# Kernel tuning notes

Hardware: AMD Instinct MI355X
Metric: run time of the kernel (lower is better)

The kernel has to match this reference:

```python
import jax, jax.numpy as jnp
import numpy as np

B, T, E, D = 8, 2048, 1024, 64  # batch, seq_len, n_emb, head_dim

def setup_inputs() -> dict:
    key = jax.random.key(0)
    ks = jax.random.split(key, 4)
    scale = 1.0 / np.sqrt(E)
    return {
        "x": jax.random.normal(ks[0], (B, T, E), dtype=jnp.float32),
        "Wq": jax.random.normal(ks[1], (E, D), dtype=jnp.float32) * scale,
        "bq": jnp.zeros((D,), dtype=jnp.float32),
        "Wk": jax.random.normal(ks[2], (E, D), dtype=jnp.float32) * scale,
        "bk": jnp.zeros((D,), dtype=jnp.float32),
        "Wv": jax.random.normal(ks[3], (E, D), dtype=jnp.float32) * scale,
        "bv": jnp.zeros((D,), dtype=jnp.float32),
    }

def reference(x, Wq, bq, Wk, bk, Wv, bv):
    # QKV projections: [B,T,E] @ [E,D] -> [B,T,D]
    q = x @ Wq + bq
    k = x @ Wk + bk
    v = x @ Wv + bv
    d = q.shape[-1]
    # scaled dot-product scores [B,T,T]
    wei = jnp.einsum('btd,bsd->bts', q, k) * (d ** -0.5)
    # causal mask: position t attends to s <= t
    t = wei.shape[1]
    causal = jnp.tril(jnp.ones((t, t), dtype=bool))
    wei = jnp.where(causal, wei, -jnp.inf)
    wei = jax.nn.softmax(wei, axis=-1)
    # attention output [B,T,D]
    return jnp.einsum('bts,bsd->btd', wei, v)
```

## Files before the change

### kernel.cpp

```cpp
#include <hip/hip_runtime.h>
#include <math.h>


#define B_   8
#define T_   2048
#define E_   1024
#define D_   64
#define BT_  (B_ * T_)

typedef __attribute__((ext_vector_type(8))) short s16x8;
typedef __attribute__((ext_vector_type(4))) short s16x4;
typedef __attribute__((ext_vector_type(4))) float f32x4;

__device__ __forceinline__ short f2bf(float f) {
    union { float f; unsigned u; } a; a.f = f;
    unsigned r = a.u + 0x7fffu + ((a.u >> 16) & 1u);
    return (short)(r >> 16);
}

#define MFMA16(a, b, c) __builtin_amdgcn_mfma_f32_16x16x32_bf16((a), (b), (c), 0, 0, 0)

#define DPPF(x, ctrl) __builtin_bit_cast(float, \
    __builtin_amdgcn_update_dpp(0, __builtin_bit_cast(int, (x)), (ctrl), 0xF, 0xF, true))

__device__ __forceinline__ float rsum16(float x) {
    x += DPPF(x, 0xB1);
    x += DPPF(x, 0x4E);
    x += DPPF(x, 0x124);
    x += DPPF(x, 0x128);
    return x;
}

__global__ __launch_bounds__(256) void wtrans_kernel(
    const float* __restrict__ Wq, const float* __restrict__ Wk,
    const float* __restrict__ Wv, short* __restrict__ Wt)
{
    __shared__ float sT[64][65];
    const int sel = blockIdx.x >> 4;
    const int k0  = (blockIdx.x & 15) * 64;
    const float* W = sel == 0 ? Wq : (sel == 1 ? Wk : Wv);
    const int t  = threadIdx.x;
    const int kr = t >> 4, c4 = (t & 15) * 4;
    #pragma unroll
    for (int i = 0; i < 4; ++i) {
        float4 v = *(const float4*)&W[(size_t)(k0 + kr + i * 16) * D_ + c4];
        sT[kr + i * 16][c4 + 0] = v.x; sT[kr + i * 16][c4 + 1] = v.y;
        sT[kr + i * 16][c4 + 2] = v.z; sT[kr + i * 16][c4 + 3] = v.w;
    }
    __syncthreads();
    #pragma unroll
    for (int i = 0; i < 4; ++i) {
        int n  = (t >> 4) + i * 16;
        int kk = (t & 15) * 4;
        s16x4 o;
        o.x = f2bf(sT[kk + 0][n]); o.y = f2bf(sT[kk + 1][n]);
        o.z = f2bf(sT[kk + 2][n]); o.w = f2bf(sT[kk + 3][n]);
        *(s16x4*)&Wt[(size_t)(sel * 64 + n) * E_ + k0 + kk] = o;
    }
}

__global__ __launch_bounds__(256) void qkv_kernel(
    const float* __restrict__ x, const short* __restrict__ Wt,
    const float* __restrict__ bq, const float* __restrict__ bk,
    const float* __restrict__ bv,
    short* __restrict__ Qg, short* __restrict__ Kg, short* __restrict__ VTg)
{
    __shared__ short sX[2][32 * 76];
    const int tid  = threadIdx.x;
    const int lane = tid & 63;
    const int w    = tid >> 6;
    const int l15  = lane & 15, quad = lane >> 4;
    const int t0   = blockIdx.x * 32;
    const int bb   = t0 >> 11;

    const int srow = tid >> 3;
    const int skc  = (tid & 7) * 8;
    const float* px = &x[(size_t)(t0 + srow) * E_ + skc];

    f32x4 acc[3][2];
    #pragma unroll
    for (int a = 0; a < 3; ++a)
        #pragma unroll
        for (int h = 0; h < 2; ++h)
            acc[a][h] = (f32x4){0.f, 0.f, 0.f, 0.f};

    float4 lda0 = *(const float4*)px;
    float4 lda1 = *(const float4*)(px + 4);
    float4 ldb0 = *(const float4*)(px + 64);
    float4 ldb1 = *(const float4*)(px + 68);

    int buf = 0;
    for (int k0 = 0; k0 < E_; k0 += 64) {
        s16x8 pk;
        pk[0] = f2bf(lda0.x); pk[1] = f2bf(lda0.y);
        pk[2] = f2bf(lda0.z); pk[3] = f2bf(lda0.w);
        pk[4] = f2bf(lda1.x); pk[5] = f2bf(lda1.y);
        pk[6] = f2bf(lda1.z); pk[7] = f2bf(lda1.w);
        *(s16x8*)&sX[buf][srow * 76 + skc] = pk;
        __syncthreads();

        lda0 = ldb0; lda1 = ldb1;
        if (k0 + 128 < E_) {
            const float* p2 = px + k0 + 128;
            ldb0 = *(const float4*)p2;
            ldb1 = *(const float4*)(p2 + 4);
        }

        s16x8 aw[3][2];
        #pragma unroll
        for (int t3 = 0; t3 < 3; ++t3) {
            const short* pw = &Wt[(size_t)((w * 3 + t3) * 16 + l15) * E_ + k0 + quad * 8];
            aw[t3][0] = *(const s16x8*)pw;
            aw[t3][1] = *(const s16x8*)(pw + 32);
        }
        s16x8 bxf[2][2];
        #pragma unroll
        for (int h = 0; h < 2; ++h) {
            bxf[h][0] = *(const s16x8*)&sX[buf][(h * 16 + l15) * 76 + quad * 8];
            bxf[h][1] = *(const s16x8*)&sX[buf][(h * 16 + l15) * 76 + 32 + quad * 8];
        }
        #pragma unroll
        for (int t3 = 0; t3 < 3; ++t3)
            #pragma unroll
            for (int h = 0; h < 2; ++h) {
                acc[t3][h] = MFMA16(aw[t3][0], bxf[h][0], acc[t3][h]);
                acc[t3][h] = MFMA16(aw[t3][1], bxf[h][1], acc[t3][h]);
            }
        buf ^= 1;
    }

    __syncthreads();
    short* sVT = &sX[0][0];

    #pragma unroll
    for (int t3 = 0; t3 < 3; ++t3) {
        const int nt = w * 3 + t3;
        const int fb = (nt & 3) * 16 + quad * 4;
        const float* bias = nt < 4 ? bq : (nt < 8 ? bk : bv);
        f32x4 bsv = *(const f32x4*)&bias[fb];
        #pragma unroll
        for (int h = 0; h < 2; ++h) {
            const int tok = t0 + h * 16 + l15;
            f32x4 v = acc[t3][h] + bsv;
            if (nt < 4) {
                v *= 0.125f;
                s16x4 o = { f2bf(v[0]), f2bf(v[1]), f2bf(v[2]), f2bf(v[3]) };
                *(s16x4*)&Qg[(size_t)tok * D_ + fb] = o;
            } else if (nt < 8) {
                s16x4 o = { f2bf(v[0]), f2bf(v[1]), f2bf(v[2]), f2bf(v[3]) };
                *(s16x4*)&Kg[(size_t)tok * D_ + fb] = o;
            } else {
                const int lt = h * 16 + l15;
                #pragma unroll
                for (int r = 0; r < 4; ++r)
                    sVT[(fb + r) * 48 + lt] = f2bf(v[r]);
            }
        }
    }
    __syncthreads();
    {
        const int d  = tid >> 2;
        const int tq = (tid & 3) * 8;
        s16x8 vv = *(const s16x8*)&sVT[d * 48 + tq];
        *(s16x8*)&VTg[(size_t)(bb * D_ + d) * T_ + (t0 & (T_ - 1)) + tq] = vv;
    }
}

__global__ __launch_bounds__(256) void attn_kernel(
    const short* __restrict__ Qg, const short* __restrict__ Kg,
    const short* __restrict__ VTg, float* __restrict__ out)
{
    __shared__ char smem[20736];
    short* sP = (short*)smem;
    float* sO = (float*)smem;
    float* sl = (float*)(smem + 20480);

    const int tid  = threadIdx.x;
    const int lane = tid & 63;
    const int w    = tid >> 6;
    const int l15  = lane & 15, quad = lane >> 4;
    const int b    = blockIdx.x & 7;
    const int pr   = blockIdx.x >> 3;
    const int jA   = pr, jB = 127 - pr;
    const int tqA  = jA * 16, tqB = jB * 16;
    const int nchA = (jA >> 2) + 1, nchB = (jB >> 2) + 1;
    const int tot  = nchA + nchB;
    const int seg  = (tot + 3) >> 2;
    const int c0   = w * seg;
    const int c1   = (c0 + seg < tot) ? c0 + seg : tot;

    const size_t qoffA = ((size_t)b * T_ + tqA + l15) * D_ + quad * 8;
    const s16x8 aqA0 = *(const s16x8*)&Qg[qoffA];
    const s16x8 aqA1 = *(const s16x8*)&Qg[qoffA + 32];
    const size_t qoffB = ((size_t)b * T_ + tqB + l15) * D_ + quad * 8;
    const s16x8 aqB0 = *(const s16x8*)&Qg[qoffB];
    const s16x8 aqB1 = *(const s16x8*)&Qg[qoffB + 32];

    f32x4 oA[4], oB[4];
    float lA[4] = {0.f, 0.f, 0.f, 0.f}, lB[4] = {0.f, 0.f, 0.f, 0.f};
    #pragma unroll
    for (int nt = 0; nt < 4; ++nt) {
        oA[nt] = (f32x4){0.f, 0.f, 0.f, 0.f};
        oB[nt] = (f32x4){0.f, 0.f, 0.f, 0.f};
    }

    const short* kb = Kg  + (size_t)b * T_ * D_;
    const short* vb = VTg + (size_t)b * D_ * T_;
    short* sPw = sP + w * (16 * 72);

    auto body = [&](int cc, int tq, int nch, const s16x8& q0, const s16x8& q1,
                    f32x4 (&oo)[4], float (&lp)[4]) {
        const int s0 = cc * 64;
        s16x8 bk[4][2];
        #pragma unroll
        for (int nt = 0; nt < 4; ++nt) {
            const short* pk = kb + (size_t)(s0 + nt * 16 + l15) * D_ + quad * 8;
            bk[nt][0] = *(const s16x8*)pk;
            bk[nt][1] = *(const s16x8*)(pk + 32);
        }
        const f32x4 zz = (f32x4){0.f, 0.f, 0.f, 0.f};
        f32x4 sacc[4];
        #pragma unroll
        for (int nt = 0; nt < 4; ++nt) {
            sacc[nt] = MFMA16(q0, bk[nt][0], zz);
            sacc[nt] = MFMA16(q1, bk[nt][1], sacc[nt]);
        }
        s16x8 bv[4][2];
        #pragma unroll
        for (int nt = 0; nt < 4; ++nt) {
            const short* pv = vb + (size_t)(nt * 16 + l15) * T_ + s0 + quad * 8;
            bv[nt][0] = *(const s16x8*)pv;
            bv[nt][1] = *(const s16x8*)(pv + 32);
        }
        const bool diag = (cc == nch - 1);
        float p[4][4];
        #pragma unroll
        for (int nt = 0; nt < 4; ++nt)
            #pragma unroll
            for (int r = 0; r < 4; ++r) {
                float e = __expf(sacc[nt][r]);
                if (diag && (s0 + nt * 16 + l15 > tq + quad * 4 + r)) e = 0.f;
                p[nt][r] = e;
            }
        #pragma unroll
        for (int r = 0; r < 4; ++r)
            lp[r] += (p[0][r] + p[1][r]) + (p[2][r] + p[3][r]);
        #pragma unroll
        for (int nt = 0; nt < 4; ++nt)
            #pragma unroll
            for (int r = 0; r < 4; ++r)
                sPw[(quad * 4 + r) * 72 + nt * 16 + l15] = f2bf(p[nt][r]);
        s16x8 ap0 = *(const s16x8*)&sPw[l15 * 72 + quad * 8];
        s16x8 ap1 = *(const s16x8*)&sPw[l15 * 72 + 32 + quad * 8];
        #pragma unroll
        for (int nt = 0; nt < 4; ++nt) {
            oo[nt] = MFMA16(ap0, bv[nt][0], oo[nt]);
            oo[nt] = MFMA16(ap1, bv[nt][1], oo[nt]);
        }
    };

    for (int c = c0; c < c1; ++c) {
        if (c < nchA) body(c, tqA, nchA, aqA0, aqA1, oA, lA);
        else          body(c - nchA, tqB, nchB, aqB0, aqB1, oB, lB);
    }

    f32x4 lvA, lvB;
    #pragma unroll
    for (int r = 0; r < 4; ++r) { lvA[r] = rsum16(lA[r]); lvB[r] = rsum16(lB[r]); }

    const int d  = tid & 63;
    const int rb = (tid >> 6) * 4;

    __syncthreads();
    {
        float* sOw = sO + w * (64 * 20);
        #pragma unroll
        for (int nt = 0; nt < 4; ++nt)
            *(f32x4*)&sOw[(nt * 16 + l15) * 20 + quad * 4] = oA[nt];
        if (l15 == 0) *(f32x4*)&sl[w * 16 + quad * 4] = lvA;
    }
    __syncthreads();
    {
        f32x4 osum = (f32x4){0.f, 0.f, 0.f, 0.f};
        f32x4 lsum = (f32x4){0.f, 0.f, 0.f, 0.f};
        #pragma unroll
        for (int w2 = 0; w2 < 4; ++w2) {
            osum += *(const f32x4*)&sO[w2 * (64 * 20) + d * 20 + rb];
            lsum += *(const f32x4*)&sl[w2 * 16 + rb];
        }
        #pragma unroll
        for (int i = 0; i < 4; ++i)
            out[((size_t)b * T_ + tqA + rb + i) * D_ + d] = osum[i] / lsum[i];
    }

    __syncthreads();
    {
        float* sOw = sO + w * (64 * 20);
        #pragma unroll
        for (int nt = 0; nt < 4; ++nt)
            *(f32x4*)&sOw[(nt * 16 + l15) * 20 + quad * 4] = oB[nt];
        if (l15 == 0) *(f32x4*)&sl[w * 16 + quad * 4] = lvB;
    }
    __syncthreads();
    {
        f32x4 osum = (f32x4){0.f, 0.f, 0.f, 0.f};
        f32x4 lsum = (f32x4){0.f, 0.f, 0.f, 0.f};
        #pragma unroll
        for (int w2 = 0; w2 < 4; ++w2) {
            osum += *(const f32x4*)&sO[w2 * (64 * 20) + d * 20 + rb];
            lsum += *(const f32x4*)&sl[w2 * 16 + rb];
        }
        #pragma unroll
        for (int i = 0; i < 4; ++i)
            out[((size_t)b * T_ + tqB + rb + i) * D_ + d] = osum[i] / lsum[i];
    }
}

extern "C" void kernel_launch(void* const* d_in, const int* in_sizes, int n_in,
                              void* d_out, int out_size, void* d_ws, size_t ws_size,
                              hipStream_t stream) {
    (void)in_sizes; (void)n_in; (void)out_size; (void)ws_size;
    const float* x  = (const float*)d_in[0];
    const float* Wq = (const float*)d_in[1];
    const float* bq = (const float*)d_in[2];
    const float* Wk = (const float*)d_in[3];
    const float* bk = (const float*)d_in[4];
    const float* Wv = (const float*)d_in[5];
    const float* bv = (const float*)d_in[6];

    char* ws = (char*)d_ws;
    short* Qg  = (short*)(ws);
    short* Kg  = (short*)(ws + (size_t)2 * 1024 * 1024);
    short* VTg = (short*)(ws + (size_t)4 * 1024 * 1024);
    short* Wt  = (short*)(ws + (size_t)6 * 1024 * 1024);

    wtrans_kernel<<<48, 256, 0, stream>>>(Wq, Wk, Wv, Wt);
    qkv_kernel<<<BT_ / 32, 256, 0, stream>>>(x, Wt, bq, bk, bv, Qg, Kg, VTg);
    attn_kernel<<<B_ * 64, 256, 0, stream>>>(Qg, Kg, VTg, (float*)d_out);
}
```

Measured before the change: 160.7 us.

## Load x fragments directly into registers in QKV projection, drop LDS staging

The QKV projection kernel now processes 16 tokens per block instead of 32. Each lane loads its x fragment straight from global memory in the MFMA operand layout, which removes the shared-memory staging of x and the per-iteration block barrier. The grid doubles and launch bounds request higher occupancy, aiming for more latency hiding. The cost is that each block reads the weight tile for half as many tokens, doubling total weight traffic, though that traffic mostly hits cache.

```diff
diff --git a/kernel.cpp b/kernel.cpp
--- a/kernel.cpp
+++ b/kernel.cpp
@@ -59,78 +59,71 @@
     }
 }
 
-__global__ __launch_bounds__(256) void qkv_kernel(
+__global__ __launch_bounds__(256, 4) void qkv_kernel(
     const float* __restrict__ x, const short* __restrict__ Wt,
     const float* __restrict__ bq, const float* __restrict__ bk,
     const float* __restrict__ bv,
     short* __restrict__ Qg, short* __restrict__ Kg, short* __restrict__ VTg)
 {
-    __shared__ short sX[2][32 * 76];
+    __shared__ short sVT[64 * 24];
     const int tid  = threadIdx.x;
     const int lane = tid & 63;
     const int w    = tid >> 6;
     const int l15  = lane & 15, quad = lane >> 4;
-    const int t0   = blockIdx.x * 32;
+    const int t0   = blockIdx.x * 16;
     const int bb   = t0 >> 11;
 
-    const int srow = tid >> 3;
-    const int skc  = (tid & 7) * 8;
-    const float* px = &x[(size_t)(t0 + srow) * E_ + skc];
-
-    f32x4 acc[3][2];
-    #pragma unroll
-    for (int a = 0; a < 3; ++a)
-        #pragma unroll
-        for (int h = 0; h < 2; ++h)
-            acc[a][h] = (f32x4){0.f, 0.f, 0.f, 0.f};
-
-    float4 lda0 = *(const float4*)px;
-    float4 lda1 = *(const float4*)(px + 4);
-    float4 ldb0 = *(const float4*)(px + 64);
-    float4 ldb1 = *(const float4*)(px + 68);
-
-    int buf = 0;
+    const float* px = &x[(size_t)(t0 + l15) * E_ + quad * 8];
+
+    f32x4 acc[3];
+    #pragma unroll
+    for (int t3 = 0; t3 < 3; ++t3) acc[t3] = (f32x4){0.f, 0.f, 0.f, 0.f};
+
+    float4 a0 = *(const float4*)(px +   0);
+    float4 a1 = *(const float4*)(px +   4);
+    float4 a2 = *(const float4*)(px +  32);
+    float4 a3 = *(const float4*)(px +  36);
+    float4 b0 = *(const float4*)(px +  64);
+    float4 b1 = *(const float4*)(px +  68);
+    float4 b2 = *(const float4*)(px +  96);
+    float4 b3 = *(const float4*)(px + 100);
+
+    const short* pw0 = &Wt[(size_t)((w * 3 + 0) * 16 + l15) * E_ + quad * 8];
+    const short* pw1 = pw0 + (size_t)16 * E_;
+    const short* pw2 = pw1 + (size_t)16 * E_;
+
     for (int k0 = 0; k0 < E_; k0 += 64) {
-        s16x8 pk;
-        pk[0] = f2bf(lda0.x); pk[1] = f2bf(lda0.y);
-        pk[2] = f2bf(lda0.z); pk[3] = f2bf(lda0.w);
-        pk[4] = f2bf(lda1.x); pk[5] = f2bf(lda1.y);
-        pk[6] = f2bf(lda1.z); pk[7] = f2bf(lda1.w);
-        *(s16x8*)&sX[buf][srow * 76 + skc] = pk;
-        __syncthreads();
-
-        lda0 = ldb0; lda1 = ldb1;
+        s16x8 f0, f1;
+        f0[0] = f2bf(a0.x); f0[1] = f2bf(a0.y); f0[2] = f2bf(a0.z); f0[3] = f2bf(a0.w);
+        f0[4] = f2bf(a1.x); f0[5] = f2bf(a1.y); f0[6] = f2bf(a1.z); f0[7] = f2bf(a1.w);
+        f1[0] = f2bf(a2.x); f1[1] = f2bf(a2.y); f1[2] = f2bf(a2.z); f1[3] = f2bf(a2.w);
+        f1[4] = f2bf(a3.x); f1[5] = f2bf(a3.y); f1[6] = f2bf(a3.z); f1[7] = f2bf(a3.w);
+
+        a0 = b0; a1 = b1; a2 = b2; a3 = b3;
         if (k0 + 128 < E_) {
             const float* p2 = px + k0 + 128;
-            ldb0 = *(const float4*)p2;
-            ldb1 = *(const float4*)(p2 + 4);
-        }
-
-        s16x8 aw[3][2];
-        #pragma unroll
-        for (int t3 = 0; t3 < 3; ++t3) {
-            const short* pw = &Wt[(size_t)((w * 3 + t3) * 16 + l15) * E_ + k0 + quad * 8];
-            aw[t3][0] = *(const s16x8*)pw;
-            aw[t3][1] = *(const s16x8*)(pw + 32);
-        }
-        s16x8 bxf[2][2];
-        #pragma unroll
-        for (int h = 0; h < 2; ++h) {
-            bxf[h][0] = *(const s16x8*)&sX[buf][(h * 16 + l15) * 76 + quad * 8];
-            bxf[h][1] = *(const s16x8*)&sX[buf][(h * 16 + l15) * 76 + 32 + quad * 8];
-        }
-        #pragma unroll
-        for (int t3 = 0; t3 < 3; ++t3)
-            #pragma unroll
-            for (int h = 0; h < 2; ++h) {
-                acc[t3][h] = MFMA16(aw[t3][0], bxf[h][0], acc[t3][h]);
-                acc[t3][h] = MFMA16(aw[t3][1], bxf[h][1], acc[t3][h]);
-            }
-        buf ^= 1;
-    }
-
-    __syncthreads();
-    short* sVT = &sX[0][0];
+            b0 = *(const float4*)(p2 +  0);
+            b1 = *(const float4*)(p2 +  4);
+            b2 = *(const float4*)(p2 + 32);
+            b3 = *(const float4*)(p2 + 36);
+        }
+
+        s16x8 aw00 = *(const s16x8*)(pw0);
+        s16x8 aw01 = *(const s16x8*)(pw0 + 32);
+        s16x8 aw10 = *(const s16x8*)(pw1);
+        s16x8 aw11 = *(const s16x8*)(pw1 + 32);
+        s16x8 aw20 = *(const s16x8*)(pw2);
+        s16x8 aw21 = *(const s16x8*)(pw2 + 32);
+
+        acc[0] = MFMA16(aw00, f0, acc[0]);
+        acc[0] = MFMA16(aw01, f1, acc[0]);
+        acc[1] = MFMA16(aw10, f0, acc[1]);
+        acc[1] = MFMA16(aw11, f1, acc[1]);
+        acc[2] = MFMA16(aw20, f0, acc[2]);
+        acc[2] = MFMA16(aw21, f1, acc[2]);
+
+        pw0 += 64; pw1 += 64; pw2 += 64;
+    }
 
     #pragma unroll
     for (int t3 = 0; t3 < 3; ++t3) {
@@ -138,31 +131,27 @@
         const int fb = (nt & 3) * 16 + quad * 4;
         const float* bias = nt < 4 ? bq : (nt < 8 ? bk : bv);
         f32x4 bsv = *(const f32x4*)&bias[fb];
-        #pragma unroll
-        for (int h = 0; h < 2; ++h) {
-            const int tok = t0 + h * 16 + l15;
-            f32x4 v = acc[t3][h] + bsv;
-            if (nt < 4) {
-                v *= 0.125f;
-                s16x4 o = { f2bf(v[0]), f2bf(v[1]), f2bf(v[2]), f2bf(v[3]) };
-                *(s16x4*)&Qg[(size_t)tok * D_ + fb] = o;
-            } else if (nt < 8) {
-                s16x4 o = { f2bf(v[0]), f2bf(v[1]), f2bf(v[2]), f2bf(v[3]) };
-                *(s16x4*)&Kg[(size_t)tok * D_ + fb] = o;
-            } else {
-                const int lt = h * 16 + l15;
-                #pragma unroll
-                for (int r = 0; r < 4; ++r)
-                    sVT[(fb + r) * 48 + lt] = f2bf(v[r]);
-            }
+        const int tok = t0 + l15;
+        f32x4 v = acc[t3] + bsv;
+        if (nt < 4) {
+            v *= 0.125f;
+            s16x4 o = { f2bf(v[0]), f2bf(v[1]), f2bf(v[2]), f2bf(v[3]) };
+            *(s16x4*)&Qg[(size_t)tok * D_ + fb] = o;
+        } else if (nt < 8) {
+            s16x4 o = { f2bf(v[0]), f2bf(v[1]), f2bf(v[2]), f2bf(v[3]) };
+            *(s16x4*)&Kg[(size_t)tok * D_ + fb] = o;
+        } else {
+            #pragma unroll
+            for (int r = 0; r < 4; ++r)
+                sVT[(fb + r) * 24 + l15] = f2bf(v[r]);
         }
     }
     __syncthreads();
     {
         const int d  = tid >> 2;
-        const int tq = (tid & 3) * 8;
-        s16x8 vv = *(const s16x8*)&sVT[d * 48 + tq];
-        *(s16x8*)&VTg[(size_t)(bb * D_ + d) * T_ + (t0 & (T_ - 1)) + tq] = vv;
+        const int tq = (tid & 3) * 4;
+        s16x4 vv = *(const s16x4*)&sVT[d * 24 + tq];
+        *(s16x4*)&VTg[(size_t)(bb * D_ + d) * T_ + (t0 & (T_ - 1)) + tq] = vv;
     }
 }
 
@@ -335,6 +324,6 @@
     short* Wt  = (short*)(ws + (size_t)6 * 1024 * 1024);
 
     wtrans_kernel<<<48, 256, 0, stream>>>(Wq, Wk, Wv, Wt);
-    qkv_kernel<<<BT_ / 32, 256, 0, stream>>>(x, Wt, bq, bk, bv, Qg, Kg, VTg);
+    qkv_kernel<<<BT_ / 16, 256, 0, stream>>>(x, Wt, bq, bk, bv, Qg, Kg, VTg);
     attn_kernel<<<B_ * 64, 256, 0, stream>>>(Qg, Kg, VTg, (float*)d_out);
 }
```

After: 200.3 us. 24.7% more time.
